# Kernel tuning notes

Hardware: AMD Instinct MI355X
Metric: run time of the kernel (lower is better)

The kernel has to match this reference:

```python
import jax, jax.numpy as jnp
import numpy as np

HID, OUT, HEADS, DIM_HEAD, TOPK, CHUNK = 512, 5, 8, 64, 8, 32
INNER = HEADS * DIM_HEAD  # 512
EPS = 1e-5


def setup_inputs():
    key = jax.random.key(0)
    ks = jax.random.split(key, 12)
    def p(k, shape, fan_in):
        return (jax.random.normal(k, shape, jnp.float32) / np.sqrt(fan_in).astype(np.float32))
    return {
        'x': jax.random.normal(ks[0], (32, 3, 32, 32), jnp.float32),
        'queries': jax.random.normal(ks[1], (4, 128, HID), jnp.float32),
        'memories': jax.random.normal(ks[2], (4, 20000, HID), jnp.float32),
        'mask': jnp.ones((4, 20000), bool),
        'conv1_w': p(ks[3], (16, 3, 3, 3), 27), 'conv1_b': jnp.zeros((16,), jnp.float32),
        'conv2_w': p(ks[4], (32, 16, 3, 3), 144), 'conv2_b': jnp.zeros((32,), jnp.float32),
        'fc1_w': p(ks[5], (32 * 8 * 8, HID), 2048), 'fc1_b': jnp.zeros((HID,), jnp.float32),
        'sq_w': p(ks[6], (HID, HID), HID), 'sq_b': jnp.zeros((HID,), jnp.float32),
        'sk_w': p(ks[7], (HID, HID), HID), 'sk_b': jnp.zeros((HID,), jnp.float32),
        'q_w': p(ks[8], (HID, INNER), HID),
        'kv_w': p(ks[9], (HID, 2 * INNER), HID),
        'out_w': p(ks[10], (INNER, HID), INNER), 'out_b': jnp.zeros((HID,), jnp.float32),
        'fc2_w': p(ks[11], (HID, OUT), HID), 'fc2_b': jnp.zeros((OUT,), jnp.float32),
    }


def _maxpool2(h):
    return jax.lax.reduce_window(h, -jnp.inf, jax.lax.max, (1, 1, 2, 2), (1, 1, 2, 2), 'VALID')


def _forward(x, queries, memories, mask, conv1_w, conv1_b, conv2_w, conv2_b,
             fc1_w, fc1_b, sq_w, sq_b, sk_w, sk_b, q_w, kv_w, out_w, out_b, fc2_w, fc2_b):
    # --- CNN branch: faithfully computed, but its output is discarded by the
    # original forward (x is overwritten by the attention output) ---
    dn = ('NCHW', 'OIHW', 'NCHW')
    h = jax.lax.conv_general_dilated(x, conv1_w, (1, 1), 'SAME', dimension_numbers=dn)
    h = _maxpool2(jax.nn.relu(h + conv1_b[None, :, None, None]))
    h = jax.lax.conv_general_dilated(h, conv2_w, (1, 1), 'SAME', dimension_numbers=dn)
    h = _maxpool2(jax.nn.relu(h + conv2_b[None, :, None, None]))
    h = h.reshape(h.shape[0], -1) @ fc1_w + fc1_b  # (B, 512), dead value (matches torch code)
    _ = h

    # --- HTMAttention ---
    b, qn, dim = queries.shape
    scale = dim ** -0.5  # chunk-scoring scale uses full dim
    mem = memories.reshape(b, -1, CHUNK, dim)            # (b, n, c, d)
    mk = mask.reshape(b, -1, CHUNK)                      # (b, n, c)

    # masked mean-pool summaries per chunk
    denom = mk.sum(-1, keepdims=True).astype(mem.dtype)  # (b, n, 1)
    summarized = jnp.where(mk[..., None], mem, 0.0).sum(2) / (denom + EPS)  # (b, n, d)

    sq = queries @ sq_w + sq_b                           # (b, i, d)
    sk = jax.lax.stop_gradient(summarized) @ sk_w + sk_b # (b, n, d)
    logits = jnp.einsum('bid,bnd->bin', sq, sk) * scale  # (b, i, n)
    neg = -jnp.finfo(logits.dtype).max
    logits = jnp.where(mk.any(-1)[:, None, :], logits, neg)

    topk_logits, topk_idx = jax.lax.top_k(logits, TOPK)  # (b, i, k)
    weights = jax.nn.softmax(topk_logits, axis=-1)       # (b, i, k)

    bidx = jnp.arange(b)[:, None, None]
    selected = mem[bidx, topk_idx]                       # (b, i, k, c, d) gather of chunks
    sel_mask = mk[bidx, topk_idx]                        # (b, i, k, c)

    # sinusoidal position over chunk positions (reversed arange, step-2 freqs)
    inv_freqs = 1e4 ** (-jnp.arange(0, dim, 2.0) / dim)              # (d/2,)
    sinu = jnp.arange(CHUNK - 1, -1, -1.0)[:, None] * inv_freqs      # (c, d/2)
    pos = jnp.concatenate([jnp.sin(sinu), jnp.cos(sinu)], -1)        # (c, d)
    selected = selected + pos

    # within-chunk multi-head attention (memories detached, as in original)
    mems_in = jax.lax.stop_gradient(selected)
    q = (queries @ q_w).reshape(b, qn, HEADS, DIM_HEAD) * (DIM_HEAD ** -0.5)  # (b,i,h,e)
    kv = (mems_in @ kv_w).reshape(b, qn, TOPK, CHUNK, 2, HEADS, DIM_HEAD)
    kk, vv = kv[..., 0, :, :], kv[..., 1, :, :]          # (b,i,k,c,h,e)

    sim = jnp.einsum('bihe,bikche->bhikc', q, kk)        # (b,h,i,k,c)
    sim = jnp.where(sel_mask[:, None], sim, neg)
    attn = jax.nn.softmax(sim, axis=-1)
    o = jnp.einsum('bhikc,bikche->bikhe', attn, vv).reshape(b, qn, TOPK, INNER)
    o = o @ out_w + out_b                                # (b, i, k, d)

    htm = (o * weights[..., None]).sum(2)                # (b, i, d)
    return htm @ fc2_w + fc2_b                           # (b, i, OUT)


def reference(x, queries, memories, mask, conv1_w, conv1_b, conv2_w, conv2_b,
              fc1_w, fc1_b, sq_w, sq_b, sk_w, sk_b, q_w, kv_w, out_w, out_b, fc2_w, fc2_b):
    return _forward(x, queries, memories, mask, conv1_w, conv1_b, conv2_w, conv2_b,
                    fc1_w, fc1_b, sq_w, sq_b, sk_w, sk_b, q_w, kv_w, out_w, out_b, fc2_w, fc2_b)
```

## Files before the change

### kernel.cpp

```cpp
#include <hip/hip_runtime.h>
#include <hip/hip_bf16.h>
#include <float.h>
#include <math.h>

#define NB      4
#define QN      128
#define HID     512
#define NMEM    20000
#define MPAD    20096
#define NCHUNK  625
#define CHUNK   32
#define HEADS   8
#define DHEAD   64
#define TOPKK   8
#define NKV     1024
#define GLD     64
#define LOGIT_SCALE 0.044194173824159216f
#define W2LD    576
#define STROWS  520
#define LGLD    640
#define TLD     4096

typedef __attribute__((ext_vector_type(8))) short bf16x8;
typedef __attribute__((ext_vector_type(4))) short bf16x4;
typedef __attribute__((ext_vector_type(4))) float f32x4;

__device__ __forceinline__ short f2bf(float f){
  __hip_bfloat16 h = __float2bfloat16(f);
  return *reinterpret_cast<short*>(&h);
}
__device__ __forceinline__ float bf2f(unsigned short s){
  __hip_bfloat16 h;
  *reinterpret_cast<unsigned short*>(&h) = s;
  return __bfloat162float(h);
}
__device__ __forceinline__ bool mask_at(const void* m, int flag, long i){
  return flag ? (((const unsigned char*)m)[i] != 0)
              : (((const int*)m)[i] != 0);
}
__device__ __forceinline__ void gload16(const void* g, void* l){
  __builtin_amdgcn_global_load_lds((const __attribute__((address_space(1))) void*)g,
                                   (__attribute__((address_space(3))) void*)l, 16, 0, 0);
}

__global__ __launch_bounds__(256) void bigsetup_kernel(const float* __restrict__ skw,
                                                       const void* __restrict__ mask,
                                                       const float* __restrict__ out_w,
                                                       const float* __restrict__ out_b,
                                                       const float* __restrict__ fc2_w,
                                                       const float* __restrict__ fc2_b,
                                                       const float* __restrict__ sq_w,
                                                       const float* __restrict__ sq_b,
                                                       const float* __restrict__ sk_b,
                                                       const float* __restrict__ q_w,
                                                       const float* __restrict__ kvw,
                                                       const float* __restrict__ queries,
                                                       float* __restrict__ skwT,
                                                       float* __restrict__ pos,
                                                       int* __restrict__ flagp,
                                                       float* __restrict__ Wf,
                                                       float* __restrict__ bfold,
                                                       float* __restrict__ W2buf,
                                                       float* __restrict__ v2,
                                                       float* __restrict__ gbuf,
                                                       unsigned short* __restrict__ wqk,
                                                       unsigned short* __restrict__ qb){
  __shared__ float sm[12480];
  int sub = blockIdx.x;
  int t = threadIdx.x;
  if (sub < 64){
    float (*tile)[65] = (float(*)[65])sm;
    int c = t & 63, rbase = t >> 6;
    int e0 = (sub >> 3) * 64, j0 = (sub & 7) * 64;
#pragma unroll
    for (int j = 0; j < 16; ++j){
      int r = rbase + j * 4;
      tile[r][c] = skw[(long)(e0 + r) * 512 + j0 + c];
    }
    __syncthreads();
#pragma unroll
    for (int j = 0; j < 16; ++j){
      int rj = rbase + j * 4;
      skwT[(long)(j0 + rj) * 512 + e0 + c] = tile[c][rj];
    }
  } else if (sub < 128){
    int s = sub - 64;
    int cc = s >> 1;
    int d = (s & 1) * 256 + t;
    int j = (d < 256) ? d : d - 256;
    float invf = expf(-((2.0f * (float)j) / 512.0f) * 9.2103403719761836f);
    float arg = (float)(31 - cc) * invf;
    pos[cc * 512 + d] = (d < 256) ? sinf(arg) : cosf(arg);
    if (s == 0 && t == 0){
      const unsigned char* mb = (const unsigned char*)mask;
      *flagp = (mb[1] != 0) ? 1 : 0;
    }
  } else if (sub < 138){
    int s = sub - 128;
    int j = s >> 1;
    int d = (s & 1) * 256 + t;
    const float4* owr = (const float4*)(out_w + (long)d * 512);
    float acc = 0.f;
    for (int k4 = 0; k4 < 128; ++k4){
      float4 a = owr[k4];
      int k = k4 * 4;
      acc += a.x * fc2_w[k * 5 + j] + a.y * fc2_w[(k + 1) * 5 + j]
           + a.z * fc2_w[(k + 2) * 5 + j] + a.w * fc2_w[(k + 3) * 5 + j];
    }
    Wf[d * 5 + j] = acc;
    if (d == 0){
      float sb = 0.f;
      for (int k = 0; k < 512; ++k) sb += out_b[k] * fc2_w[k * 5 + j];
      bfold[j] = sb + fc2_b[j];
    }
  } else if (sub < 143){
    int s = sub - 138;
    if (s < 2){
      int d = s * 256 + t;
      float acc = 0.f;
      for (int j = 0; j < 512; ++j) acc += sq_w[(long)d * 512 + j] * sk_b[j];
      W2buf[(long)d * W2LD + 512] = acc;
      for (int cc = 513; cc < W2LD; ++cc) W2buf[(long)d * W2LD + cc] = 0.f;
    } else if (s < 4){
      int e = (s - 2) * 256 + t;
      float acc = 0.f;
      for (int j = 0; j < 512; ++j) acc += skw[(long)e * 512 + j] * sq_b[j];
      v2[e] = acc;
    } else {
      __shared__ float g[256];
      g[t] = sq_b[t] * sk_b[t] + sq_b[t + 256] * sk_b[t + 256];
      __syncthreads();
      for (int d = 128; d >= 1; d >>= 1){
        if (t < d) g[t] += g[t + d];
        __syncthreads();
      }
      if (t == 0) gbuf[0] = g[0];
    }
  } else if (sub < 399){
    int bx = sub - 143;
    int h = bx >> 5, rem2 = bx & 31, dp = rem2 >> 2, dd = rem2 & 3;
    int dpr0 = dp * 64, dd0 = dd * 128;
    float (*Akv)[65] = (float(*)[65])sm;
    float (*Bq)[65]  = (float(*)[65])(sm + 64 * 65);
    for (int idx = t; idx < 64 * 64; idx += 256){
      int r = idx >> 6, e = idx & 63;
      Akv[r][e] = kvw[(long)(dpr0 + r) * NKV + h * 64 + e];
    }
    for (int idx = t; idx < 128 * 64; idx += 256){
      int r = idx >> 6, e = idx & 63;
      Bq[r][e] = q_w[(long)(dd0 + r) * 512 + h * 64 + e];
    }
    __syncthreads();
    int ty = t >> 4, tx = t & 15;
    float acc[4][8] = {};
    for (int e = 0; e < 64; ++e){
      float a0 = Akv[ty * 4 + 0][e], a1 = Akv[ty * 4 + 1][e];
      float a2 = Akv[ty * 4 + 2][e], a3 = Akv[ty * 4 + 3][e];
      float b[8];
#pragma unroll
      for (int v = 0; v < 8; ++v) b[v] = Bq[tx * 8 + v][e];
#pragma unroll
      for (int v = 0; v < 8; ++v){
        acc[0][v] += a0 * b[v];
        acc[1][v] += a1 * b[v];
        acc[2][v] += a2 * b[v];
        acc[3][v] += a3 * b[v];
      }
    }
#pragma unroll
    for (int u = 0; u < 4; ++u)
#pragma unroll
      for (int v = 0; v < 8; ++v)
        wqk[(long)(h * 512 + dpr0 + ty * 4 + u) * 512 + dd0 + tx * 8 + v] =
            (unsigned short)f2bf(acc[u][v] * 0.125f);
  } else {
    long idx = (long)(sub - 399) * 256 + t;
    float4 v = *(const float4*)(queries + idx * 4);
    ushort4 o;
    o.x = (unsigned short)f2bf(v.x);
    o.y = (unsigned short)f2bf(v.y);
    o.z = (unsigned short)f2bf(v.z);
    o.w = (unsigned short)f2bf(v.w);
    *(ushort4*)(qb + idx * 4) = o;
  }
}

__global__ __launch_bounds__(512) void psetup_kernel(const float* __restrict__ kvw,
                                                     const float* __restrict__ Wf,
                                                     unsigned short* __restrict__ PB){
  int row = blockIdx.x;
  int d = threadIdx.x;
  unsigned short v = 0;
  if (row < 40){
    int h = row / 5, j = row - h * 5;
    const float* kr = kvw + (long)d * NKV + 512 + h * 64;
    const float* wr = Wf + (long)(h * 64) * 5 + j;
    float s = 0.f;
#pragma unroll
    for (int e = 0; e < 64; ++e) s += kr[e] * wr[e * 5];
    v = (unsigned short)f2bf(s);
  }
  PB[(long)row * 512 + d] = v;
}

__global__ __launch_bounds__(256) void gemm_nn2(const float* __restrict__ A, int lda,
                                                const float* __restrict__ B, int ldb,
                                                float* __restrict__ C, int ldc,
                                                int K, float scale){
  int tid = threadIdx.x;
  int lane = tid & 63, w = tid >> 6;
  int r0 = blockIdx.x * 8 + w * 2;
  int n  = blockIdx.y * 64 + lane;
  const float* a0 = A + (long)r0 * lda;
  const float* bp = B + n;
  float acc0 = 0.f, acc1 = 0.f;
#pragma unroll 4
  for (int k = 0; k < K; k += 4){
    float b0 = bp[(long)k * ldb];
    float b1 = bp[(long)(k + 1) * ldb];
    float b2 = bp[(long)(k + 2) * ldb];
    float b3 = bp[(long)(k + 3) * ldb];
    float4 a;
    a = *(const float4*)(a0 + k);
    acc0 += a.x * b0 + a.y * b1 + a.z * b2 + a.w * b3;
    a = *(const float4*)(a0 + lda + k);
    acc1 += a.x * b0 + a.y * b1 + a.z * b2 + a.w * b3;
  }
  C[(long)r0 * ldc + n]       = acc0 * scale;
  C[(long)(r0 + 1) * ldc + n] = acc1 * scale;
}

__global__ __launch_bounds__(512) void prepsum_kernel(const float* __restrict__ memories,
                                                      const float* __restrict__ pos,
                                                      const void* __restrict__ mask,
                                                      const int* __restrict__ flagp,
                                                      unsigned short* __restrict__ abf_all,
                                                      float* __restrict__ summ,
                                                      float* __restrict__ chunkden){
  int n = blockIdx.x, b = blockIdx.y;
  int t = threadIdx.x;
  unsigned short* abf = abf_all + (long)b * MPAD * 512;
  if (n == NCHUNK){
    for (int idx = t; idx < 96 * 128; idx += 512){
      ushort4 z = {0, 0, 0, 0};
      *(ushort4*)(abf + (long)(NMEM + (idx >> 7)) * 512 + (long)(idx & 127) * 4) = z;
    }
    return;
  }
  long mbase = (long)b * NMEM + (long)n * CHUNK;
  int flag = *flagp;
  bool mybit = mask_at(mask, flag, mbase + (t & 31));
  unsigned int m32 = (unsigned int)__ballot(mybit);
  float den = (float)__popc(m32);
  int rh = t >> 6;
  int c8 = t & 63;
  const float* base = memories + mbase * HID + c8 * 8;
  const float* pbase = pos + c8 * 8;
  float4 va[4], vb[4], pa[4], pb[4];
#pragma unroll
  for (int j = 0; j < 4; ++j){
    va[j] = *(const float4*)(base + (long)(rh + 8 * j) * HID);
    vb[j] = *(const float4*)(base + (long)(rh + 8 * j) * HID + 4);
  }
#pragma unroll
  for (int j = 0; j < 4; ++j){
    pa[j] = *(const float4*)(pbase + (rh + 8 * j) * HID);
    pb[j] = *(const float4*)(pbase + (rh + 8 * j) * HID + 4);
  }
#pragma unroll
  for (int j = 0; j < 4; ++j){
    union { unsigned short u[8]; int4 v; } o;
    o.u[0] = (unsigned short)f2bf(va[j].x + pa[j].x);
    o.u[1] = (unsigned short)f2bf(va[j].y + pa[j].y);
    o.u[2] = (unsigned short)f2bf(va[j].z + pa[j].z);
    o.u[3] = (unsigned short)f2bf(va[j].w + pa[j].w);
    o.u[4] = (unsigned short)f2bf(vb[j].x + pb[j].x);
    o.u[5] = (unsigned short)f2bf(vb[j].y + pb[j].y);
    o.u[6] = (unsigned short)f2bf(vb[j].z + pb[j].z);
    o.u[7] = (unsigned short)f2bf(vb[j].w + pb[j].w);
    *(int4*)(abf + (long)(n * CHUNK + rh + 8 * j) * 512 + c8 * 8) = o.v;
  }
  float acc[8] = {};
#pragma unroll
  for (int j = 0; j < 4; ++j){
    if (m32 & (1u << (rh + 8 * j))){
      acc[0] += va[j].x; acc[1] += va[j].y; acc[2] += va[j].z; acc[3] += va[j].w;
      acc[4] += vb[j].x; acc[5] += vb[j].y; acc[6] += vb[j].z; acc[7] += vb[j].w;
    }
  }
  __shared__ float red[512][9];
#pragma unroll
  for (int k = 0; k < 8; ++k) red[t][k] = acc[k];
  __syncthreads();
  if (rh == 0){
    float s[8] = {};
    for (int g = 0; g < 8; ++g)
#pragma unroll
      for (int k = 0; k < 8; ++k) s[k] += red[g * 64 + c8][k];
    float dv = den + 1e-5f;
    float4 s0 = {s[0] / dv, s[1] / dv, s[2] / dv, s[3] / dv};
    float4 s1 = {s[4] / dv, s[5] / dv, s[6] / dv, s[7] / dv};
    float* srow = summ + ((long)b * NCHUNK + n) * 512 + c8 * 8;
    *(float4*)srow = s0;
    *(float4*)(srow + 4) = s1;
    if (t == 0) chunkden[b * NCHUNK + n] = den;
  }
}

__global__ __launch_bounds__(256) void gt_gemm(const unsigned short* __restrict__ abf_all,
                                               const unsigned short* __restrict__ PB,
                                               unsigned short* __restrict__ g_all,
                                               const unsigned short* __restrict__ Aq,
                                               const unsigned short* __restrict__ Bw,
                                               float* __restrict__ T){
  __shared__ unsigned short pool[20480];
  int blk = blockIdx.x;
  int tid = threadIdx.x, wid = tid >> 6, lane = tid & 63;
  int lr = lane & 15, lg = lane >> 4;
  int scol = (lane & 3) << 3;
  int srow = wid * 16 + (lane >> 2);

  if (blk < 316){
    int bb = blk / 79, g = blk - bb * 79;
    const unsigned short* A = abf_all + (size_t)bb * MPAD * 512;
    unsigned short* gout = g_all + (size_t)bb * MPAD * GLD;
    unsigned short* As[2] = { pool, pool + 8192 };
    unsigned short* Bs[2] = { pool + 16384, pool + 18432 };
    long rbase = (long)g * 256 + srow;
    long ra0 = rbase;       if (ra0 > MPAD - 1) ra0 = MPAD - 1;
    long ra1 = rbase + 64;  if (ra1 > MPAD - 1) ra1 = MPAD - 1;
    long ra2 = rbase + 128; if (ra2 > MPAD - 1) ra2 = MPAD - 1;
    long ra3 = rbase + 192; if (ra3 > MPAD - 1) ra3 = MPAD - 1;
    const unsigned short* gA0 = A + ra0 * 512 + scol;
    const unsigned short* gA1 = A + ra1 * 512 + scol;
    const unsigned short* gA2 = A + ra2 * 512 + scol;
    const unsigned short* gA3 = A + ra3 * 512 + scol;
    const unsigned short* gB0 = PB + (long)srow * 512 + scol;
    int lA0 = (wid * 16) * 32, lA1 = (64 + wid * 16) * 32;
    int lA2 = (128 + wid * 16) * 32, lA3 = (192 + wid * 16) * 32;
    int lB0 = (wid * 16) * 32;

    f32x4 acc[4][4];
#pragma unroll
    for (int i = 0; i < 4; ++i)
#pragma unroll
      for (int j = 0; j < 4; ++j) acc[i][j] = (f32x4)0.f;

#define GSTAGE(B, K0) { gload16(gA0 + (K0), &As[B][lA0]); gload16(gA1 + (K0), &As[B][lA1]); \
                        gload16(gA2 + (K0), &As[B][lA2]); gload16(gA3 + (K0), &As[B][lA3]); \
                        gload16(gB0 + (K0), &Bs[B][lB0]); }
#define GCOMPUTE(B) { bf16x8 af[4], bfv[4]; \
  _Pragma("unroll") for (int mi = 0; mi < 4; ++mi) af[mi]  = *(const bf16x8*)&As[B][(wid * 64 + mi * 16 + lr) * 32 + lg * 8]; \
  _Pragma("unroll") for (int ni = 0; ni < 4; ++ni) bfv[ni] = *(const bf16x8*)&Bs[B][(ni * 16 + lr) * 32 + lg * 8]; \
  _Pragma("unroll") for (int mi = 0; mi < 4; ++mi) \
    _Pragma("unroll") for (int ni = 0; ni < 4; ++ni) \
      acc[mi][ni] = __builtin_amdgcn_mfma_f32_16x16x32_bf16(af[mi], bfv[ni], acc[mi][ni], 0, 0, 0); }

    GSTAGE(0, 0);
    __syncthreads();
#pragma unroll 1
    for (int tt = 0; tt < 16; tt += 2){
      if (tt + 1 < 16) GSTAGE(1, (tt + 1) * 32);
      GCOMPUTE(0);
      __syncthreads();
      if (tt + 2 < 16) GSTAGE(0, (tt + 2) * 32);
      GCOMPUTE(1);
      __syncthreads();
    }
#undef GSTAGE
#undef GCOMPUTE

#pragma unroll
    for (int mi = 0; mi < 4; ++mi)
#pragma unroll
      for (int ni = 0; ni < 4; ++ni)
#pragma unroll
        for (int rr = 0; rr < 4; ++rr){
          long gr = (long)g * 256 + wid * 64 + mi * 16 + lg * 4 + rr;
          int gn = ni * 16 + lr;
          if (gr < MPAD)
            gout[gr * GLD + gn] = (unsigned short)f2bf(acc[mi][ni][rr]);
        }
  } else {
    int L2 = blk - 316;
    int panel = L2 >> 5, nb = L2 & 31;
    int m0 = panel << 7, n0 = nb << 7;
    int wr = wid >> 1, wc = wid & 1;
    unsigned short* As[2] = { pool, pool + 4096 };
    unsigned short* Bs[2] = { pool + 8192, pool + 12288 };
    const unsigned short* gA0 = Aq + (long)(m0 + srow) * 512 + scol;
    const unsigned short* gA1 = gA0 + 64 * 512;
    const unsigned short* gB0 = Bw + (long)(n0 + srow) * 512 + scol;
    const unsigned short* gB1 = gB0 + 64 * 512;
    int lofs0 = (wid * 16) * 32;
    int lofs1 = (64 + wid * 16) * 32;

    f32x4 acc[4][4];
#pragma unroll
    for (int i = 0; i < 4; ++i)
#pragma unroll
      for (int j = 0; j < 4; ++j) acc[i][j] = (f32x4)0.f;

#define TSTAGE(B, K0) { gload16(gA0 + (K0), &As[B][lofs0]); gload16(gA1 + (K0), &As[B][lofs1]); \
                        gload16(gB0 + (K0), &Bs[B][lofs0]); gload16(gB1 + (K0), &Bs[B][lofs1]); }
#define TCOMPUTE(B) { bf16x8 af[4], bfv[4]; \
  _Pragma("unroll") for (int mi = 0; mi < 4; ++mi) af[mi]  = *(const bf16x8*)&As[B][(wr * 64 + mi * 16 + lr) * 32 + lg * 8]; \
  _Pragma("unroll") for (int ni = 0; ni < 4; ++ni) bfv[ni] = *(const bf16x8*)&Bs[B][(wc * 64 + ni * 16 + lr) * 32 + lg * 8]; \
  _Pragma("unroll") for (int mi = 0; mi < 4; ++mi) \
    _Pragma("unroll") for (int ni = 0; ni < 4; ++ni) \
      acc[mi][ni] = __builtin_amdgcn_mfma_f32_16x16x32_bf16(af[mi], bfv[ni], acc[mi][ni], 0, 0, 0); }

    TSTAGE(0, 0);
    __syncthreads();
#pragma unroll 1
    for (int tt = 0; tt < 16; tt += 2){
      if (tt + 1 < 16) TSTAGE(1, (tt + 1) * 32);
      TCOMPUTE(0);
      __syncthreads();
      if (tt + 2 < 16) TSTAGE(0, (tt + 2) * 32);
      TCOMPUTE(1);
      __syncthreads();
    }
#undef TSTAGE
#undef TCOMPUTE

#pragma unroll
    for (int mi = 0; mi < 4; ++mi)
#pragma unroll
      for (int ni = 0; ni < 4; ++ni)
#pragma unroll
        for (int rr = 0; rr < 4; ++rr){
          int gr = m0 + wr * 64 + mi * 16 + lg * 4 + rr;
          int gn = n0 + wc * 64 + ni * 16 + lr;
          T[(long)gr * TLD + gn] = acc[mi][ni][rr];
        }
  }
}

__global__ __launch_bounds__(256) void ustb_kernel(const float* __restrict__ queries,
                                                   const float* __restrict__ W2buf,
                                                   float* __restrict__ u_ext,
                                                   const float* __restrict__ summ,
                                                   const float* __restrict__ v2,
                                                   const float* __restrict__ gbuf,
                                                   float* __restrict__ summText,
                                                   float* __restrict__ betag){
  int blk = blockIdx.x;
  int t = threadIdx.x;
  if (blk < 576){
    int ax = blk & 63, ay = blk >> 6;
    int lane = t & 63, w = t >> 6;
    int r0 = ax * 8 + w * 2;
    int n  = ay * 64 + lane;
    const float* a0 = queries + (long)r0 * 512;
    const float* bp = W2buf + n;
    float acc0 = 0.f, acc1 = 0.f;
#pragma unroll 4
    for (int k = 0; k < 512; k += 4){
      float b0 = bp[(long)k * W2LD];
      float b1 = bp[(long)(k + 1) * W2LD];
      float b2 = bp[(long)(k + 2) * W2LD];
      float b3 = bp[(long)(k + 3) * W2LD];
      float4 a;
      a = *(const float4*)(a0 + k);
      acc0 += a.x * b0 + a.y * b1 + a.z * b2 + a.w * b3;
      a = *(const float4*)(a0 + 512 + k);
      acc1 += a.x * b0 + a.y * b1 + a.z * b2 + a.w * b3;
    }
    u_ext[(long)r0 * W2LD + n]       = acc0;
    u_ext[(long)(r0 + 1) * W2LD + n] = acc1;
  } else if (blk < 896){
    __shared__ float tile[64][65];
    int b2 = blk - 576;
    int b = b2 / 80; int rem = b2 % 80;
    int n0 = (rem / 8) * 64, e0 = (rem % 8) * 64;
    int c = t & 63, rbase = t >> 6;
#pragma unroll
    for (int j = 0; j < 16; ++j){
      int r = rbase + j * 4;
      int n = n0 + r;
      tile[r][c] = (n < NCHUNK) ? summ[((long)b * NCHUNK + n) * 512 + e0 + c] : 0.f;
    }
    __syncthreads();
#pragma unroll
    for (int j = 0; j < 16; ++j){
      int re = rbase + j * 4;
      summText[(long)b * STROWS * LGLD + (long)(e0 + re) * LGLD + n0 + c] = tile[c][re];
    }
  } else if (blk < 900){
    int b = blk - 896;
    for (int idx = t; idx < 8 * LGLD; idx += 256){
      int e = idx / LGLD, n = idx - e * LGLD;
      summText[(long)b * STROWS * LGLD + (long)(512 + e) * LGLD + n] = (e == 0) ? 1.f : 0.f;
    }
  } else {
    int bb = blk - 900;
    int w = t >> 6, lane = t & 63;
    int row = bb * 4 + w;
    const float* r = summ + (long)row * 512;
    float s = 0.f;
#pragma unroll
    for (int c = 0; c < 8; ++c) s += r[lane + 64 * c] * v2[lane + 64 * c];
    for (int d = 32; d >= 1; d >>= 1) s += __shfl_xor(s, d, 64);
    if (lane == 0){
      int b = row / NCHUNK, n = row % NCHUNK;
      betag[b * LGLD + n] = s + gbuf[0];
    }
  }
}

__global__ __launch_bounds__(256) void logits_nn(const float* __restrict__ u_ext,
                                                 const float* __restrict__ summText,
                                                 const float* __restrict__ betag,
                                                 const float* __restrict__ chunkden,
                                                 float* __restrict__ logits){
  int b = blockIdx.z;
  int tid = threadIdx.x;
  int lane = tid & 63, w = tid >> 6;
  int r0 = blockIdx.x * 8 + w * 2;
  int n  = blockIdx.y * 64 + lane;
  const float* a0 = u_ext + ((long)b * QN + r0) * W2LD;
  const float* bp = summText + (long)b * STROWS * LGLD + n;
  float acc0 = 0.f, acc1 = 0.f;
#pragma unroll 4
  for (int k = 0; k < STROWS; k += 4){
    float b0 = bp[(long)k * LGLD];
    float b1 = bp[(long)(k + 1) * LGLD];
    float b2 = bp[(long)(k + 2) * LGLD];
    float b3 = bp[(long)(k + 3) * LGLD];
    float4 a;
    a = *(const float4*)(a0 + k);
    acc0 += a.x * b0 + a.y * b1 + a.z * b2 + a.w * b3;
    a = *(const float4*)(a0 + W2LD + k);
    acc1 += a.x * b0 + a.y * b1 + a.z * b2 + a.w * b3;
  }
  if (n < NCHUNK){
    float bet = betag[b * LGLD + n];
    bool dead = (chunkden[b * NCHUNK + n] <= 0.f);
    float v0 = (acc0 + bet) * LOGIT_SCALE;
    float v1 = (acc1 + bet) * LOGIT_SCALE;
    if (dead){ v0 = v1 = -FLT_MAX; }
    long base = ((long)b * QN + r0) * LGLD + n;
    logits[base]        = v0;
    logits[base + LGLD] = v1;
  }
}

__global__ __launch_bounds__(256) void topk_kernel(const float* __restrict__ logits,
                                                   int* __restrict__ topi_out,
                                                   float* __restrict__ wts_out){
  int row = blockIdx.x;
  __shared__ float lds[NCHUNK];
  __shared__ float wv[4];
  __shared__ int   wi[4];
  __shared__ float topv[TOPKK];
  __shared__ int   topi[TOPKK];
  int t = threadIdx.x;
  int lane = t & 63, w = t >> 6;
  for (int idx = t; idx < NCHUNK; idx += 256) lds[idx] = logits[(long)row * LGLD + idx];
  __syncthreads();
  for (int it = 0; it < TOPKK; ++it){
    float bv = -INFINITY; int bi = 0x7fffffff;
    for (int idx = t; idx < NCHUNK; idx += 256){
      float v = lds[idx];
      if (v > bv){ bv = v; bi = idx; }
    }
    for (int d = 32; d >= 1; d >>= 1){
      float ov = __shfl_xor(bv, d, 64);
      int   oi = __shfl_xor(bi, d, 64);
      if (ov > bv || (ov == bv && oi < bi)){ bv = ov; bi = oi; }
    }
    if (lane == 0){ wv[w] = bv; wi[w] = bi; }
    __syncthreads();
    if (t == 0){
      float fb = wv[0]; int fi = wi[0];
      for (int j = 1; j < 4; ++j){
        if (wv[j] > fb || (wv[j] == fb && wi[j] < fi)){ fb = wv[j]; fi = wi[j]; }
      }
      topv[it] = fb; topi[it] = fi; lds[fi] = -INFINITY;
    }
    __syncthreads();
  }
  if (t == 0){
    float m = topv[0];
    for (int r = 1; r < TOPKK; ++r) m = fmaxf(m, topv[r]);
    float e[TOPKK], s = 0.f;
    for (int r = 0; r < TOPKK; ++r){ e[r] = expf(topv[r] - m); s += e[r]; }
    for (int r = 0; r < TOPKK; ++r){
      wts_out[(long)row * TOPKK + r] = e[r] / s;
      topi_out[(long)row * TOPKK + r] = topi[r];
    }
  }
}

#define ALDP 516
__global__ __launch_bounds__(256) void attn5_kernel(const float* __restrict__ T,
                                                    const unsigned short* __restrict__ abf_all,
                                                    const unsigned short* __restrict__ g_all,
                                                    const int* __restrict__ topidx,
                                                    const float* __restrict__ wts,
                                                    const void* __restrict__ mask,
                                                    const int* __restrict__ flagp,
                                                    float* __restrict__ osc5){
  int bx = blockIdx.x;
  int bb = bx >> 10, rem = bx & 1023;
  int i = rem >> 3, k = rem & 7;
  const unsigned short* abf = abf_all + (size_t)bb * MPAD * 512;
  const unsigned short* gb  = g_all + (size_t)bb * MPAD * GLD;
  int t = threadIdx.x;
  __shared__ unsigned short A_lds[32 * ALDP];
  __shared__ float T_lds[TLD];
  __shared__ float red[4][5];
  int flag = *flagp;
  long sel = ((long)(bb * QN + i)) * TOPKK + k;
  int chunk = topidx[sel];
  float w8 = wts[sel];
  const float* Trow = T + (long)(bb * QN + i) * TLD;
  for (int idx = t; idx < 1024; idx += 256)
    *(float4*)&T_lds[idx * 4] = *(const float4*)&Trow[idx * 4];
  {
    int r = t >> 3, cb = (t & 7) * 64;
    const unsigned short* src = abf + (long)(chunk * CHUNK + r) * 512 + cb;
    unsigned short* dst = &A_lds[r * ALDP + cb];
#pragma unroll
    for (int j = 0; j < 8; ++j){
      bf16x8 a8 = *(const bf16x8*)(src + j * 8);
      bf16x4 lo = {a8[0], a8[1], a8[2], a8[3]};
      bf16x4 hi = {a8[4], a8[5], a8[6], a8[7]};
      *(bf16x4*)(dst + j * 8)     = lo;
      *(bf16x4*)(dst + j * 8 + 4) = hi;
    }
  }
  __syncthreads();
  int h = t >> 5, c = t & 31;
  const unsigned short* arow = &A_lds[c * ALDP];
  const float* tp = &T_lds[h * 512];
  float s = 0.f;
#pragma unroll 4
  for (int e8 = 0; e8 < 64; ++e8){
    bf16x4 alo = *(const bf16x4*)(arow + e8 * 8);
    bf16x4 ahi = *(const bf16x4*)(arow + e8 * 8 + 4);
    float4 ta = *(const float4*)(tp + e8 * 8);
    float4 tb = *(const float4*)(tp + e8 * 8 + 4);
    s += bf2f((unsigned short)alo[0]) * ta.x + bf2f((unsigned short)alo[1]) * ta.y
       + bf2f((unsigned short)alo[2]) * ta.z + bf2f((unsigned short)alo[3]) * ta.w
       + bf2f((unsigned short)ahi[0]) * tb.x + bf2f((unsigned short)ahi[1]) * tb.y
       + bf2f((unsigned short)ahi[2]) * tb.z + bf2f((unsigned short)ahi[3]) * tb.w;
  }
  bool mv = mask_at(mask, flag, (long)bb * NMEM + (long)chunk * CHUNK + c);
  if (!mv) s = -FLT_MAX;
  float m = s;
  for (int d = 16; d >= 1; d >>= 1) m = fmaxf(m, __shfl_xor(m, d, 32));
  float p = expf(s - m);
  float su = p;
  for (int d = 16; d >= 1; d >>= 1) su += __shfl_xor(su, d, 32);
  float att = p / su;
  const unsigned short* grow = gb + (long)(chunk * CHUNK + c) * GLD + h * 5;
  float p0 = att * bf2f(grow[0]);
  float p1 = att * bf2f(grow[1]);
  float p2 = att * bf2f(grow[2]);
  float p3 = att * bf2f(grow[3]);
  float p4 = att * bf2f(grow[4]);
#pragma unroll
  for (int d = 32; d >= 1; d >>= 1){
    p0 += __shfl_xor(p0, d, 64);
    p1 += __shfl_xor(p1, d, 64);
    p2 += __shfl_xor(p2, d, 64);
    p3 += __shfl_xor(p3, d, 64);
    p4 += __shfl_xor(p4, d, 64);
  }
  int w = t >> 6, lane = t & 63;
  if (lane == 0){
    red[w][0] = p0; red[w][1] = p1; red[w][2] = p2; red[w][3] = p3; red[w][4] = p4;
  }
  __syncthreads();
  if (t < 5){
    float tot = red[0][t] + red[1][t] + red[2][t] + red[3][t];
    osc5[sel * 8 + t] = w8 * tot;
  }
}

__global__ __launch_bounds__(64) void final5_kernel(const float* __restrict__ osc5,
                                                    const float* __restrict__ bfold,
                                                    float* __restrict__ out){
  int bi = blockIdx.x;
  int t = threadIdx.x;
  if (t < 5){
    float a = bfold[t];
#pragma unroll
    for (int k = 0; k < TOPKK; ++k) a += osc5[((long)bi * TOPKK + k) * 8 + t];
    out[bi * 5 + t] = a;
  }
}

extern "C" void kernel_launch(void* const* d_in, const int* in_sizes, int n_in,
                              void* d_out, int out_size, void* d_ws, size_t ws_size,
                              hipStream_t stream) {
  const float* queries  = (const float*)d_in[1];
  const float* memories = (const float*)d_in[2];
  const void*  mask     = d_in[3];
  const float* sq_w = (const float*)d_in[10];
  const float* sq_b = (const float*)d_in[11];
  const float* sk_w = (const float*)d_in[12];
  const float* sk_b = (const float*)d_in[13];
  const float* q_w  = (const float*)d_in[14];
  const float* kv_w = (const float*)d_in[15];
  const float* out_w = (const float*)d_in[16];
  const float* out_b = (const float*)d_in[17];
  const float* fc2_w = (const float*)d_in[18];
  const float* fc2_b = (const float*)d_in[19];
  float* out = (float*)d_out;

  char* ws = (char*)d_ws;
  size_t off = 0;
  auto alloc = [&](size_t bytes){ size_t o = off; off += (bytes + 511) & ~(size_t)511; return o; };
  size_t o_sum  = alloc(5120000);
  size_t o_den  = alloc(10240);
  size_t o_pos  = alloc(65536);
  size_t o_wf   = alloc(10240);
  size_t o_bf   = alloc(512);
  size_t o_ti   = alloc(16384);
  size_t o_wt   = alloc(16384);
  size_t o_flag = alloc(512);
  size_t o_w2   = alloc(1179648);
  size_t o_uex  = alloc(1179648);
  size_t o_st   = alloc(5324800);
  size_t o_bg   = alloc(10240);
  size_t o_v2   = alloc(2048);
  size_t o_gm   = alloc(512);
  size_t o_lg   = alloc(1310720);
  size_t o_osc5 = alloc(131072);
  size_t o_skt  = alloc(1048576);
  size_t o_qbf  = alloc(524288);
  size_t o_wqk  = alloc(4194304);
  size_t o_T    = alloc((size_t)NB * QN * TLD * 4);
  size_t o_pb   = alloc(65536);
  size_t o_abf  = alloc((size_t)NB * MPAD * 512 * 2);
  size_t o_g    = alloc((size_t)NB * MPAD * GLD * 2);

  float* summ  = (float*)(ws + o_sum);
  float* den   = (float*)(ws + o_den);
  float* pos   = (float*)(ws + o_pos);
  float* Wf    = (float*)(ws + o_wf);
  float* bfold = (float*)(ws + o_bf);
  int*   ti    = (int*)  (ws + o_ti);
  float* wt    = (float*)(ws + o_wt);
  int*   flagp = (int*)  (ws + o_flag);
  float* W2buf = (float*)(ws + o_w2);
  float* u_ext = (float*)(ws + o_uex);
  float* summText = (float*)(ws + o_st);
  float* betag = (float*)(ws + o_bg);
  float* v2    = (float*)(ws + o_v2);
  float* gbuf  = (float*)(ws + o_gm);
  float* logit = (float*)(ws + o_lg);
  float* osc5  = (float*)(ws + o_osc5);
  float* skwT  = (float*)(ws + o_skt);
  unsigned short* qb   = (unsigned short*)(ws + o_qbf);
  unsigned short* wqk  = (unsigned short*)(ws + o_wqk);
  float* Tbuf  = (float*)(ws + o_T);
  unsigned short* PB   = (unsigned short*)(ws + o_pb);
  unsigned short* abf  = (unsigned short*)(ws + o_abf);
  unsigned short* gall = (unsigned short*)(ws + o_g);

  bigsetup_kernel<<<dim3(655), dim3(256), 0, stream>>>(
      sk_w, mask, out_w, out_b, fc2_w, fc2_b, sq_w, sq_b, sk_b, q_w, kv_w, queries,
      skwT, pos, flagp, Wf, bfold, W2buf, v2, gbuf, wqk, qb);
  psetup_kernel<<<dim3(64), dim3(512), 0, stream>>>(kv_w, Wf, PB);
  gemm_nn2<<<dim3(64, 8), dim3(256), 0, stream>>>(sq_w, 512, skwT, 512, W2buf, W2LD, 512, 1.0f);

  prepsum_kernel<<<dim3(NCHUNK + 1, NB), dim3(512), 0, stream>>>(
      memories, pos, mask, flagp, abf, summ, den);

  gt_gemm<<<dim3(444), dim3(256), 0, stream>>>(abf, PB, gall, qb, wqk, Tbuf);

  ustb_kernel<<<dim3(1525), dim3(256), 0, stream>>>(
      queries, W2buf, u_ext, summ, v2, gbuf, summText, betag);
  logits_nn<<<dim3(16, 10, NB), dim3(256), 0, stream>>>(u_ext, summText, betag, den, logit);
  topk_kernel<<<dim3(NB * QN), dim3(256), 0, stream>>>(logit, ti, wt);

  attn5_kernel<<<dim3(NB * QN * TOPKK), dim3(256), 0, stream>>>(
      Tbuf, abf, gall, ti, wt, mask, flagp, osc5);
  final5_kernel<<<dim3(NB * QN), dim3(64), 0, stream>>>(osc5, bfold, out);
}
```

Baseline: 310.1 us.

## Fold psetup into bigsetup and gemm_nn2 into gt_gemm launch

Removes two separate kernel launches. The Wf/PB setup is merged into bigsetup as extra blocks, each recomputing its 64-entry slice of out_w·fc2_w in shared memory. The sq_w·skwT GEMM that fills W2buf becomes 512 extra blocks appended to gt_gemm. This cuts launch overhead and serialization, but adds redundant per-block work and makes gt_gemm heterogeneous.

```diff
diff --git a/kernel.cpp b/kernel.cpp
--- a/kernel.cpp
+++ b/kernel.cpp
@@ -58,13 +58,13 @@
                                                        float* __restrict__ skwT,
                                                        float* __restrict__ pos,
                                                        int* __restrict__ flagp,
-                                                       float* __restrict__ Wf,
                                                        float* __restrict__ bfold,
                                                        float* __restrict__ W2buf,
                                                        float* __restrict__ v2,
                                                        float* __restrict__ gbuf,
                                                        unsigned short* __restrict__ wqk,
-                                                       unsigned short* __restrict__ qb){
+                                                       unsigned short* __restrict__ qb,
+                                                       unsigned short* __restrict__ PB){
   __shared__ float sm[12480];
   int sub = blockIdx.x;
   int t = threadIdx.x;
@@ -95,26 +95,14 @@
       const unsigned char* mb = (const unsigned char*)mask;
       *flagp = (mb[1] != 0) ? 1 : 0;
     }
-  } else if (sub < 138){
-    int s = sub - 128;
-    int j = s >> 1;
-    int d = (s & 1) * 256 + t;
-    const float4* owr = (const float4*)(out_w + (long)d * 512);
-    float acc = 0.f;
-    for (int k4 = 0; k4 < 128; ++k4){
-      float4 a = owr[k4];
-      int k = k4 * 4;
-      acc += a.x * fc2_w[k * 5 + j] + a.y * fc2_w[(k + 1) * 5 + j]
-           + a.z * fc2_w[(k + 2) * 5 + j] + a.w * fc2_w[(k + 3) * 5 + j];
-    }
-    Wf[d * 5 + j] = acc;
-    if (d == 0){
+  } else if (sub == 128){
+    if (t < 5){
       float sb = 0.f;
-      for (int k = 0; k < 512; ++k) sb += out_b[k] * fc2_w[k * 5 + j];
-      bfold[j] = sb + fc2_b[j];
-    }
-  } else if (sub < 143){
-    int s = sub - 138;
+      for (int k = 0; k < 512; ++k) sb += out_b[k] * fc2_w[k * 5 + t];
+      bfold[t] = sb + fc2_b[t];
+    }
+  } else if (sub < 134){
+    int s = sub - 129;
     if (s < 2){
       int d = s * 256 + t;
       float acc = 0.f;
@@ -136,8 +124,8 @@
       }
       if (t == 0) gbuf[0] = g[0];
     }
-  } else if (sub < 399){
-    int bx = sub - 143;
+  } else if (sub < 390){
+    int bx = sub - 134;
     int h = bx >> 5, rem2 = bx & 31, dp = rem2 >> 2, dd = rem2 & 3;
     int dpr0 = dp * 64, dd0 = dd * 128;
     float (*Akv)[65] = (float(*)[65])sm;
@@ -173,8 +161,8 @@
       for (int v = 0; v < 8; ++v)
         wqk[(long)(h * 512 + dpr0 + ty * 4 + u) * 512 + dd0 + tx * 8 + v] =
             (unsigned short)f2bf(acc[u][v] * 0.125f);
-  } else {
-    long idx = (long)(sub - 399) * 256 + t;
+  } else if (sub < 646){
+    long idx = (long)(sub - 390) * 256 + t;
     float4 v = *(const float4*)(queries + idx * 4);
     ushort4 o;
     o.x = (unsigned short)f2bf(v.x);
@@ -182,52 +170,29 @@
     o.z = (unsigned short)f2bf(v.z);
     o.w = (unsigned short)f2bf(v.w);
     *(ushort4*)(qb + idx * 4) = o;
-  }
-}
-
-__global__ __launch_bounds__(512) void psetup_kernel(const float* __restrict__ kvw,
-                                                     const float* __restrict__ Wf,
-                                                     unsigned short* __restrict__ PB){
-  int row = blockIdx.x;
-  int d = threadIdx.x;
-  unsigned short v = 0;
-  if (row < 40){
-    int h = row / 5, j = row - h * 5;
-    const float* kr = kvw + (long)d * NKV + 512 + h * 64;
-    const float* wr = Wf + (long)(h * 64) * 5 + j;
-    float s = 0.f;
-#pragma unroll
-    for (int e = 0; e < 64; ++e) s += kr[e] * wr[e * 5];
-    v = (unsigned short)f2bf(s);
-  }
-  PB[(long)row * 512 + d] = v;
-}
-
-__global__ __launch_bounds__(256) void gemm_nn2(const float* __restrict__ A, int lda,
-                                                const float* __restrict__ B, int ldb,
-                                                float* __restrict__ C, int ldc,
-                                                int K, float scale){
-  int tid = threadIdx.x;
-  int lane = tid & 63, w = tid >> 6;
-  int r0 = blockIdx.x * 8 + w * 2;
-  int n  = blockIdx.y * 64 + lane;
-  const float* a0 = A + (long)r0 * lda;
-  const float* bp = B + n;
-  float acc0 = 0.f, acc1 = 0.f;
-#pragma unroll 4
-  for (int k = 0; k < K; k += 4){
-    float b0 = bp[(long)k * ldb];
-    float b1 = bp[(long)(k + 1) * ldb];
-    float b2 = bp[(long)(k + 2) * ldb];
-    float b3 = bp[(long)(k + 3) * ldb];
-    float4 a;
-    a = *(const float4*)(a0 + k);
-    acc0 += a.x * b0 + a.y * b1 + a.z * b2 + a.w * b3;
-    a = *(const float4*)(a0 + lda + k);
-    acc1 += a.x * b0 + a.y * b1 + a.z * b2 + a.w * b3;
-  }
-  C[(long)r0 * ldc + n]       = acc0 * scale;
-  C[(long)(r0 + 1) * ldc + n] = acc1 * scale;
+  } else {
+    int row = sub - 646;
+    if (row < 40){
+      int h = row / 5, j = row - h * 5;
+      __shared__ float wfc[64];
+      if (t < 64){
+        const float* owr = out_w + (long)(h * 64 + t) * 512;
+        float s = 0.f;
+        for (int k = 0; k < 512; ++k) s += owr[k] * fc2_w[k * 5 + j];
+        wfc[t] = s;
+      }
+      __syncthreads();
+      for (int d = t; d < 512; d += 256){
+        const float* kr = kvw + (long)d * NKV + 512 + h * 64;
+        float s = 0.f;
+#pragma unroll
+        for (int e = 0; e < 64; ++e) s += kr[e] * wfc[e];
+        PB[(long)row * 512 + d] = (unsigned short)f2bf(s);
+      }
+    } else {
+      for (int d = t; d < 512; d += 256) PB[(long)row * 512 + d] = 0;
+    }
+  }
 }
 
 __global__ __launch_bounds__(512) void prepsum_kernel(const float* __restrict__ memories,
@@ -312,7 +277,10 @@
                                                unsigned short* __restrict__ g_all,
                                                const unsigned short* __restrict__ Aq,
                                                const unsigned short* __restrict__ Bw,
-                                               float* __restrict__ T){
+                                               float* __restrict__ T,
+                                               const float* __restrict__ sq_w,
+                                               const float* __restrict__ skwT,
+                                               float* __restrict__ W2buf){
   __shared__ unsigned short pool[20480];
   int blk = blockIdx.x;
   int tid = threadIdx.x, wid = tid >> 6, lane = tid & 63;
@@ -381,7 +349,7 @@
           if (gr < MPAD)
             gout[gr * GLD + gn] = (unsigned short)f2bf(acc[mi][ni][rr]);
         }
-  } else {
+  } else if (blk < 444){
     int L2 = blk - 316;
     int panel = L2 >> 5, nb = L2 & 31;
     int m0 = panel << 7, n0 = nb << 7;
@@ -434,6 +402,28 @@
           int gn = n0 + wc * 64 + ni * 16 + lr;
           T[(long)gr * TLD + gn] = acc[mi][ni][rr];
         }
+  } else {
+    int bx3 = blk - 444;
+    int rt = bx3 & 63, nt2 = bx3 >> 6;
+    int r0 = rt * 8 + wid * 2;
+    int nn = nt2 * 64 + lane;
+    const float* a0 = sq_w + (long)r0 * 512;
+    const float* bp = skwT + nn;
+    float acc0 = 0.f, acc1 = 0.f;
+#pragma unroll 4
+    for (int k = 0; k < 512; k += 4){
+      float b0 = bp[(long)k * 512];
+      float b1 = bp[(long)(k + 1) * 512];
+      float b2 = bp[(long)(k + 2) * 512];
+      float b3 = bp[(long)(k + 3) * 512];
+      float4 a;
+      a = *(const float4*)(a0 + k);
+      acc0 += a.x * b0 + a.y * b1 + a.z * b2 + a.w * b3;
+      a = *(const float4*)(a0 + 512 + k);
+      acc1 += a.x * b0 + a.y * b1 + a.z * b2 + a.w * b3;
+    }
+    W2buf[(long)r0 * W2LD + nn]       = acc0;
+    W2buf[(long)(r0 + 1) * W2LD + nn] = acc1;
   }
 }
 
@@ -717,7 +707,6 @@
   size_t o_sum  = alloc(5120000);
   size_t o_den  = alloc(10240);
   size_t o_pos  = alloc(65536);
-  size_t o_wf   = alloc(10240);
   size_t o_bf   = alloc(512);
   size_t o_ti   = alloc(16384);
   size_t o_wt   = alloc(16384);
@@ -741,7 +730,6 @@
   float* summ  = (float*)(ws + o_sum);
   float* den   = (float*)(ws + o_den);
   float* pos   = (float*)(ws + o_pos);
-  float* Wf    = (float*)(ws + o_wf);
   float* bfold = (float*)(ws + o_bf);
   int*   ti    = (int*)  (ws + o_ti);
   float* wt    = (float*)(ws + o_wt);
@@ -762,16 +750,15 @@
   unsigned short* abf  = (unsigned short*)(ws + o_abf);
   unsigned short* gall = (unsigned short*)(ws + o_g);
 
-  bigsetup_kernel<<<dim3(655), dim3(256), 0, stream>>>(
+  bigsetup_kernel<<<dim3(710), dim3(256), 0, stream>>>(
       sk_w, mask, out_w, out_b, fc2_w, fc2_b, sq_w, sq_b, sk_b, q_w, kv_w, queries,
-      skwT, pos, flagp, Wf, bfold, W2buf, v2, gbuf, wqk, qb);
-  psetup_kernel<<<dim3(64), dim3(512), 0, stream>>>(kv_w, Wf, PB);
-  gemm_nn2<<<dim3(64, 8), dim3(256), 0, stream>>>(sq_w, 512, skwT, 512, W2buf, W2LD, 512, 1.0f);
+      skwT, pos, flagp, bfold, W2buf, v2, gbuf, wqk, qb, PB);
 
   prepsum_kernel<<<dim3(NCHUNK + 1, NB), dim3(512), 0, stream>>>(
       memories, pos, mask, flagp, abf, summ, den);
 
-  gt_gemm<<<dim3(444), dim3(256), 0, stream>>>(abf, PB, gall, qb, wqk, Tbuf);
+  gt_gemm<<<dim3(956), dim3(256), 0, stream>>>(
+      abf, PB, gall, qb, wqk, Tbuf, sq_w, skwT, W2buf);
 
   ustb_kernel<<<dim3(1525), dim3(256), 0, stream>>>(
       queries, W2buf, u_ext, summ, v2, gbuf, summText, betag);
```

After: 275.5 us, median of 3. 11.1% less time.
